# Optimization experiments

Measured on AMD Instinct MI355X. Metric: run time of the kernel, lower is better.

The kernel has to match this reference:

```python
import jax, jax.numpy as jnp
import numpy as np

DIM_IN, DIM_OUT, DIM_INNER = 1024, 1024, 128
SCALE = DIM_INNER ** -0.5


def setup_inputs() -> dict:
    key = jax.random.key(0)
    k1, k2, k3, k4 = jax.random.split(key, 4)
    x = jax.random.normal(k1, (4, 4096, DIM_IN), dtype=jnp.float32)
    # torch nn.Linear stores weight as [out, in]; we keep that layout and transpose in matmul
    w_qkv = jax.random.normal(k2, (3 * DIM_INNER, DIM_IN), dtype=jnp.float32) * (DIM_IN ** -0.5)
    w_out = jax.random.normal(k3, (DIM_OUT, DIM_INNER), dtype=jnp.float32) * (DIM_INNER ** -0.5)
    b_out = jax.random.normal(k4, (DIM_OUT,), dtype=jnp.float32) * 0.02
    return {"x": x, "w_qkv": w_qkv, "w_out": w_out, "b_out": b_out}


def reference(x, w_qkv, w_out, b_out):
    # qkv projection (no bias)
    qkv = jnp.einsum('bnd,ed->bne', x, w_qkv)            # [b, n, 3*dim_inner]
    q, k, v = jnp.split(qkv, 3, axis=-1)                 # each [b, n, dim_inner]
    sim = jnp.einsum('bid,bjd->bij', q, k) * SCALE       # [b, n, n]
    n = sim.shape[-1]
    causal = jnp.triu(jnp.ones((n, n), dtype=bool), 1)   # True above diagonal
    neg = jnp.finfo(q.dtype).max
    sim = jnp.where(causal[None, :, :], -neg, sim)
    attn = jax.nn.softmax(sim, axis=-1)
    out = jnp.einsum('bij,bjd->bid', attn, v)            # [b, n, dim_inner]
    return jnp.einsum('bnd,od->bno', out, w_out) + b_out # [b, n, dim_out]
```

## Files before the change

### kernel.cpp

```cpp
#include <hip/hip_runtime.h>
#include <math.h>


typedef __attribute__((ext_vector_type(8))) short bf16x8;
typedef __attribute__((ext_vector_type(4))) short bf16x4;
typedef __attribute__((ext_vector_type(4))) float f32x4;

#define FA_SCL2 0.12751886525137387f

__device__ __forceinline__ unsigned short f2bf(float f) {
    __bf16 h = (__bf16)f;
    return __builtin_bit_cast(unsigned short, h);
}
__device__ __forceinline__ float bf2f(unsigned short h) {
    union { unsigned u; float f; } v; v.u = ((unsigned)h) << 16;
    return v.f;
}
__device__ __forceinline__ f32x4 mfma16(bf16x8 a, bf16x8 b, f32x4 c) {
    return __builtin_amdgcn_mfma_f32_16x16x32_bf16(a, b, c, 0, 0, 0);
}
__device__ __forceinline__ void gl2lds16(const void* g, void* l) {
    __builtin_amdgcn_global_load_lds(
        (const __attribute__((address_space(1))) unsigned int*)g,
        (__attribute__((address_space(3))) unsigned int*)l, 16, 0, 0);
}
__device__ __forceinline__ f32x4 vmax4(f32x4 a, f32x4 b) {
    return f32x4{fmaxf(a[0], b[0]), fmaxf(a[1], b[1]),
                 fmaxf(a[2], b[2]), fmaxf(a[3], b[3])};
}

__global__ __launch_bounds__(256)
void wcast(const float* __restrict__ W, unsigned short* __restrict__ wfm)
{
    const int idx = blockIdx.x * 256 + threadIdx.x;
    const int kc = idx & 127, r = idx >> 7;
    const float* g = W + (size_t)r * 1024 + kc * 8;
    float4 w0 = *(const float4*)g, w1 = *(const float4*)(g + 4);
    bf16x8 p;
    p[0] = (short)f2bf(w0.x); p[1] = (short)f2bf(w0.y);
    p[2] = (short)f2bf(w0.z); p[3] = (short)f2bf(w0.w);
    p[4] = (short)f2bf(w1.x); p[5] = (short)f2bf(w1.y);
    p[6] = (short)f2bf(w1.z); p[7] = (short)f2bf(w1.w);
    *(bf16x8*)&wfm[(size_t)(kc * 384 + r) * 8] = p;
}

__global__ __launch_bounds__(256)
void woutcast(const float* __restrict__ W, unsigned short* __restrict__ wofm)
{
    const int idx = blockIdx.x * 256 + threadIdx.x;
    const int c = idx & 15, rg = idx >> 4;
    const float* g = W + (size_t)rg * 128 + c * 8;
    float4 w0 = *(const float4*)g, w1 = *(const float4*)(g + 4);
    bf16x8 p;
    p[0] = (short)f2bf(w0.x); p[1] = (short)f2bf(w0.y);
    p[2] = (short)f2bf(w0.z); p[3] = (short)f2bf(w0.w);
    p[4] = (short)f2bf(w1.x); p[5] = (short)f2bf(w1.y);
    p[6] = (short)f2bf(w1.z); p[7] = (short)f2bf(w1.w);
    *(bf16x8*)&wofm[((size_t)((rg >> 6) * 16 + c) * 64 + (rg & 63)) * 8] = p;
}

__global__ __launch_bounds__(512)
void gemm_qkv(const float* __restrict__ X, const unsigned short* __restrict__ Wfm,
              unsigned short* __restrict__ qfm, unsigned short* __restrict__ kfm,
              unsigned short* __restrict__ vpl)
{
    __shared__ unsigned short Asl[2048];
    __shared__ unsigned short Bsl[3][12288];
    const int tid = threadIdx.x;
    const int wv = tid >> 6, lane = tid & 63;
    const int lm = lane & 15, quad = lane >> 4;
    const int mb = blockIdx.x * 64;
    const int arow = tid >> 3, af4 = tid & 7;

    f32x4 acc[4][3];
    #pragma unroll
    for (int i = 0; i < 4; ++i)
        #pragma unroll
        for (int j = 0; j < 3; ++j) acc[i][j] = f32x4{0.f, 0.f, 0.f, 0.f};

    const float* gx = X + (size_t)(mb + arow) * 1024 + af4 * 4;

    auto issueB = [&](int it, int buf) {
        #pragma unroll
        for (int i = 0; i < 3; ++i) {
            const int p = wv * 3 + i;
            const int kcl = p & 3, rg = p >> 2;
            gl2lds16(Wfm + (size_t)((it * 4 + kcl) * 384 + rg * 64) * 8 + lane * 8,
                     &Bsl[buf][(kcl * 384 + rg * 64) * 8]);
        }
    };

    float4 f0 = *(const float4*)gx;
    issueB(0, 0);
    float4 f1 = *(const float4*)(gx + 32);
    issueB(1, 1);

    auto step = [&](const int i, float4& f) {
        __builtin_amdgcn_s_barrier();
        {
            bf16x4 pk;
            pk[0] = (short)f2bf(f.x); pk[1] = (short)f2bf(f.y);
            pk[2] = (short)f2bf(f.z); pk[3] = (short)f2bf(f.w);
            *(bf16x4*)&Asl[((af4 >> 1) * 64 + arow) * 8 + (af4 & 1) * 4] = pk;
        }
        if (i < 30) {
            f = *(const float4*)(gx + (i + 2) * 32);
            issueB(i + 2, (i + 2) % 3);
            asm volatile("s_waitcnt vmcnt(14) lgkmcnt(0)" ::: "memory");
        } else if (i == 30) {
            asm volatile("s_waitcnt vmcnt(7) lgkmcnt(0)" ::: "memory");
        } else {
            asm volatile("s_waitcnt vmcnt(0) lgkmcnt(0)" ::: "memory");
        }
        __builtin_amdgcn_s_barrier();
        const unsigned short* Bc = Bsl[i % 3];
        bf16x8 afr[4], bfr[3];
        #pragma unroll
        for (int i4 = 0; i4 < 4; ++i4)
            afr[i4] = *(const bf16x8*)&Asl[(quad * 64 + i4 * 16 + lm) * 8];
        #pragma unroll
        for (int j = 0; j < 3; ++j)
            bfr[j] = *(const bf16x8*)&Bc[(quad * 384 + wv * 48 + j * 16 + lm) * 8];
        #pragma unroll
        for (int i4 = 0; i4 < 4; ++i4)
            #pragma unroll
            for (int j = 0; j < 3; ++j)
                acc[i4][j] = mfma16(afr[i4], bfr[j], acc[i4][j]);
    };

    for (int p = 0; p < 16; ++p) { step(2 * p, f0); step(2 * p + 1, f1); }

    #pragma unroll
    for (int j = 0; j < 3; ++j) {
        const int ncg = wv * 48 + j * 16 + lm;
        const int sect = ncg >> 7, ncol = ncg & 127;
        if (sect == 2) {
            #pragma unroll
            for (int i = 0; i < 4; ++i)
                #pragma unroll
                for (int r = 0; r < 4; ++r)
                    vpl[(size_t)(mb + i * 16 + quad * 4 + r) * 128 + ncol]
                        = f2bf(acc[i][j][r]);
        } else {
            unsigned short* dst = sect ? kfm : qfm;
            const float scl = sect ? 1.f : FA_SCL2;
            const size_t cb = ((size_t)blockIdx.x * 16 + (ncol >> 3)) * 512 + (ncol & 7);
            #pragma unroll
            for (int i = 0; i < 4; ++i)
                #pragma unroll
                for (int r = 0; r < 4; ++r)
                    dst[cb + (size_t)(i * 16 + quad * 4 + r) * 8]
                        = f2bf(acc[i][j][r] * scl);
        }
    }
}

__global__ __launch_bounds__(256)
void transpose_v(const unsigned short* __restrict__ V, unsigned short* __restrict__ Vfm)
{
    __shared__ unsigned short T[128 * 72];
    const int tid = threadIdx.x;
    const int b  = blockIdx.x >> 6;
    const int kt = blockIdx.x & 63;
    const unsigned short* src = V + ((size_t)b * 4096 + kt * 64) * 128;
    #pragma unroll
    for (int i = 0; i < 4; ++i) {
        const int idx = tid + i * 256;
        const int key = idx >> 4, c8 = (idx & 15) * 8;
        bf16x8 d = *(const bf16x8*)(src + key * 128 + c8);
        #pragma unroll
        for (int e = 0; e < 8; ++e) T[(c8 + e) * 72 + key] = (unsigned short)d[e];
    }
    __syncthreads();
    unsigned short* dst = Vfm + (size_t)(b * 64 + kt) * 8192;
    #pragma unroll
    for (int i = 0; i < 4; ++i) {
        const int o = tid + i * 256;
        const int d = o & 127, c = o >> 7;
        bf16x8 x = *(const bf16x8*)&T[d * 72 + c * 8];
        *(bf16x8*)(dst + ((size_t)c * 128 + d) * 8) = x;
    }
}

__global__ __launch_bounds__(512)
void flash_attn3(const unsigned short* __restrict__ Qfm, const unsigned short* __restrict__ Kfm,
                 const unsigned short* __restrict__ Vfm,
                 unsigned short* __restrict__ Opart, float* __restrict__ Ml)
{
    __shared__ unsigned short Klds[2][8192];
    __shared__ unsigned short Vlds[2][8192];
    __shared__ unsigned short Plds[8][1024];

    const int tid = threadIdx.x;
    const int wv = tid >> 6, lane = tid & 63;
    const int lm = lane & 15, quad = lane >> 4;

    const int bx = blockIdx.x;
    const int xcd = bx & 7;
    const int b   = xcd >> 1;
    const int r   = (bx >> 3) * 2 + (xcd & 1);
    const int sp  = r & 3;
    const int Qi  = (r < 64) ? (16 + (r >> 2)) : (15 - ((r - 64) >> 2));
    const int n   = 2 * Qi + 2;
    const int cnt = (n >> 2) + ((sp < (n & 3)) ? 1 : 0);
    const int ktb = sp * (n >> 2) + ((sp < (n & 3)) ? sp : (n & 3));
    const int kte = ktb + cnt;
    const int qtw = 2 * Qi + (wv >> 2);
    const int rw  = (wv & 3) * 16;

    const int qt0 = 2 * Qi;
    const size_t ob0 = (size_t)((b * 64 + qt0) * 4 + sp) * 8192;
    const size_t ob1 = ob0 + 4 * 8192;
    const int mlb0 = ((b * 64 + qt0) * 4 + sp) * 128, mlb1 = mlb0 + 512;

    if (cnt == 0) {
        bf16x8 z = {0, 0, 0, 0, 0, 0, 0, 0};
        #pragma unroll
        for (int t = 0; t < 2; ++t) {
            *(bf16x8*)&Opart[ob0 + (size_t)(tid + t * 512) * 8] = z;
            *(bf16x8*)&Opart[ob1 + (size_t)(tid + t * 512) * 8] = z;
        }
        if (tid < 64) { Ml[mlb0 + tid] = -INFINITY; Ml[mlb1 + tid] = -INFINITY; }
        else if (tid < 128) { Ml[mlb0 + tid] = 0.f; Ml[mlb1 + tid] = 0.f; }
        return;
    }

    {
        const size_t qb = (size_t)(b * 64 + qt0) * 8192;
        #pragma unroll
        for (int i = 0; i < 4; ++i) {
            const int p = wv * 4 + i;
            gl2lds16(Qfm + qb + (size_t)p * 512 + lane * 8, &Klds[0][0] + p * 512);
        }
    }
    __syncthreads();
    bf16x8 qf[4];
    {
        const unsigned short* Qt = &Klds[wv >> 2][0];
        #pragma unroll
        for (int c = 0; c < 4; ++c)
            qf[c] = *(const bf16x8*)&Qt[((c * 4 + quad) * 64 + rw + lm) * 8];
    }
    asm volatile("s_waitcnt lgkmcnt(0)" ::: "memory");
    __builtin_amdgcn_s_barrier();

    {
        const size_t kb = (size_t)(b * 64 + ktb) * 8192;
        #pragma unroll
        for (int i = 0; i < 2; ++i) {
            const int pc = wv * 2 + i;
            gl2lds16(Kfm + kb + pc * 512 + lane * 8, &Klds[0][pc * 512]);
            gl2lds16(Vfm + kb + pc * 512 + lane * 8, &Vlds[0][pc * 512]);
        }
    }

    f32x4 oacc[8];
    #pragma unroll
    for (int oc = 0; oc < 8; ++oc) oacc[oc] = f32x4{0.f, 0.f, 0.f, 0.f};
    f32x4 m4 = f32x4{-INFINITY, -INFINITY, -INFINITY, -INFINITY};
    f32x4 lacc = f32x4{0.f, 0.f, 0.f, 0.f};
    unsigned short* Pw = Plds[wv];
    const short ONE = (short)0x3F80;
    const bf16x8 ONESB = {ONE, ONE, ONE, ONE, ONE, ONE, ONE, ONE};

    for (int kt = ktb; kt < kte; ++kt) {
        const int cu = (kt - ktb) & 1;
        __builtin_amdgcn_s_barrier();
        if (kt + 1 < kte) {
            const size_t kb = (size_t)(b * 64 + kt + 1) * 8192;
            #pragma unroll
            for (int i = 0; i < 2; ++i) {
                const int pc = wv * 2 + i;
                gl2lds16(Kfm + kb + pc * 512 + lane * 8, &Klds[cu ^ 1][pc * 512]);
                gl2lds16(Vfm + kb + pc * 512 + lane * 8, &Vlds[cu ^ 1][pc * 512]);
            }
            asm volatile("s_waitcnt vmcnt(4)" ::: "memory");
        } else {
            asm volatile("s_waitcnt vmcnt(0)" ::: "memory");
        }
        __builtin_amdgcn_s_barrier();
        if (kt > qtw) continue;

        const unsigned short* Kc = &Klds[cu][0];
        const unsigned short* Vc = &Vlds[cu][0];

        f32x4 sv[4];
        __builtin_amdgcn_s_setprio(1);
        #pragma unroll
        for (int ct = 0; ct < 4; ++ct) {
            f32x4 a = f32x4{0.f, 0.f, 0.f, 0.f};
            #pragma unroll
            for (int c = 0; c < 4; ++c) {
                bf16x8 kf = *(const bf16x8*)&Kc[((c * 4 + quad) * 64 + ct * 16 + lm) * 8];
                a = mfma16(qf[c], kf, a);
            }
            sv[ct] = a;
        }
        __builtin_amdgcn_s_setprio(0);
        if (kt == qtw) {
            #pragma unroll
            for (int ct = 0; ct < 4; ++ct) {
                const int dg = ct * 16 + lm - rw - quad * 4;
                #pragma unroll
                for (int rr = 0; rr < 4; ++rr)
                    if (dg > rr) sv[ct][rr] = -INFINITY;
            }
        }
        const f32x4 pmax = vmax4(vmax4(sv[0], sv[1]), vmax4(sv[2], sv[3]));
        const float dm = fmaxf(fmaxf(pmax[0] - m4[0], pmax[1] - m4[1]),
                               fmaxf(pmax[2] - m4[2], pmax[3] - m4[3]));
        if (!__all(dm <= 8.f)) {
            f32x4 rmax = pmax;
            #pragma unroll
            for (int d = 1; d < 16; d <<= 1) {
                f32x4 o;
                #pragma unroll
                for (int e = 0; e < 4; ++e) o[e] = __shfl_xor(rmax[e], d);
                rmax = vmax4(rmax, o);
            }
            const f32x4 mnew = vmax4(m4, rmax);
            f32x4 alpha;
            #pragma unroll
            for (int e = 0; e < 4; ++e) alpha[e] = __builtin_amdgcn_exp2f(m4[e] - mnew[e]);
            m4 = mnew;
            #pragma unroll
            for (int oc = 0; oc < 8; ++oc) oacc[oc] *= alpha;
            lacc *= alpha;
        }
        #pragma unroll
        for (int ct = 0; ct < 4; ++ct)
            #pragma unroll
            for (int rr = 0; rr < 4; ++rr)
                sv[ct][rr] = __builtin_amdgcn_exp2f(sv[ct][rr] - m4[rr]);
        #pragma unroll
        for (int ct = 0; ct < 4; ++ct) {
            const int cb = ((ct * 2 + (lm >> 3)) * 16 + quad * 4) * 8 + (lm & 7);
            #pragma unroll
            for (int rr = 0; rr < 4; ++rr)
                Pw[cb + rr * 8] = f2bf(sv[ct][rr]);
        }
        __builtin_amdgcn_s_setprio(1);
        #pragma unroll
        for (int s = 0; s < 2; ++s) {
            bf16x8 pf = *(const bf16x8*)&Pw[((s * 4 + quad) * 16 + lm) * 8];
            lacc = mfma16(pf, ONESB, lacc);
            #pragma unroll
            for (int oc = 0; oc < 8; ++oc) {
                bf16x8 vf = *(const bf16x8*)&Vc[((s * 4 + quad) * 128 + oc * 16 + lm) * 8];
                oacc[oc] = mfma16(pf, vf, oacc[oc]);
            }
        }
        __builtin_amdgcn_s_setprio(0);
    }

    const size_t obw = (size_t)((b * 64 + qtw) * 4 + sp) * 8192;
    const int mlw = ((b * 64 + qtw) * 4 + sp) * 128;
    #pragma unroll
    for (int oc = 0; oc < 8; ++oc) {
        const size_t cb = obw + (size_t)((oc * 2 + (lm >> 3)) * 64
                          + rw + quad * 4) * 8 + (lm & 7);
        #pragma unroll
        for (int rr = 0; rr < 4; ++rr)
            Opart[cb + rr * 8] = f2bf(oacc[oc][rr]);
    }
    if (lm == 0)
        #pragma unroll
        for (int rr = 0; rr < 4; ++rr) {
            const int row = rw + quad * 4 + rr;
            Ml[mlw + row] = m4[rr];
            Ml[mlw + 64 + row] = lacc[rr];
        }
}

__global__ __launch_bounds__(256)
void fa_combine(const unsigned short* __restrict__ Opart, const float* __restrict__ Ml,
                unsigned short* __restrict__ Ofm)
{
    const int bq = blockIdx.x;
    const int tid = threadIdx.x;
    const size_t pbase = (size_t)bq * 4 * 8192;
    const int mlb = bq * 4 * 128;
    #pragma unroll
    for (int t = 0; t < 4; ++t) {
        const int g = tid + t * 256;
        const int r = g & 63;
        float m[4], l[4];
        #pragma unroll
        for (int s = 0; s < 4; ++s) {
            m[s] = Ml[mlb + s * 128 + r];
            l[s] = Ml[mlb + s * 128 + 64 + r];
        }
        const float M = fmaxf(fmaxf(m[0], m[1]), fmaxf(m[2], m[3]));
        float a[4], den = 0.f;
        #pragma unroll
        for (int s = 0; s < 4; ++s) {
            a[s] = __builtin_amdgcn_exp2f(m[s] - M);
            den += a[s] * l[s];
        }
        const float rsc = 1.f / den;
        float acc[8] = {};
        #pragma unroll
        for (int s = 0; s < 4; ++s) {
            bf16x8 x = *(const bf16x8*)&Opart[pbase + (size_t)s * 8192 + (size_t)g * 8];
            #pragma unroll
            for (int e = 0; e < 8; ++e) acc[e] += a[s] * bf2f((unsigned short)x[e]);
        }
        bf16x8 o;
        #pragma unroll
        for (int e = 0; e < 8; ++e) o[e] = f2bf(acc[e] * rsc);
        *(bf16x8*)&Ofm[(size_t)bq * 8192 + (size_t)g * 8] = o;
    }
}

__global__ __launch_bounds__(256)
void gemm_out(const unsigned short* __restrict__ Ain, const unsigned short* __restrict__ Wofm,
              const float* __restrict__ bias, float* __restrict__ out)
{
    __shared__ unsigned short Bsl[16384];
    __shared__ unsigned short Asl[2][4096];
    const int tid = threadIdx.x;
    const int mb = blockIdx.x * 128;
    const int nb = blockIdx.y * 128;
    const int wv = tid >> 6, lane = tid & 63;
    const int wr = (wv >> 1) * 64, wc = (wv & 1) * 64;
    const int lm = lane & 15, quad = lane >> 4;

    #pragma unroll
    for (int i = 0; i < 8; ++i) {
        const int p = wv * 8 + i;
        gl2lds16(Wofm + (size_t)(((nb >> 6) + (p >> 4)) * 16 + (p & 15)) * 512 + lane * 8,
                 &Bsl[p * 512]);
    }
    #pragma unroll
    for (int i = 0; i < 2; ++i) {
        const int id = wv * 2 + i, t = id >> 2, kcl = id & 3;
        gl2lds16(Ain + (size_t)((mb >> 6) + t) * 8192 + kcl * 512 + lane * 8,
                 &Asl[0][(t * 4 + kcl) * 512]);
    }

    f32x4 acc[4][4];
    #pragma unroll
    for (int i = 0; i < 4; ++i)
        #pragma unroll
        for (int j = 0; j < 4; ++j) acc[i][j] = f32x4{0.f, 0.f, 0.f, 0.f};

    for (int kt = 0; kt < 4; ++kt) {
        __builtin_amdgcn_s_barrier();
        if (kt < 3) {
            #pragma unroll
            for (int i = 0; i < 2; ++i) {
                const int id = wv * 2 + i, t = id >> 2, kcl = id & 3;
                gl2lds16(Ain + (size_t)((mb >> 6) + t) * 8192 + ((kt + 1) * 4 + kcl) * 512 + lane * 8,
                         &Asl[(kt + 1) & 1][(t * 4 + kcl) * 512]);
            }
            asm volatile("s_waitcnt vmcnt(2)" ::: "memory");
        } else {
            asm volatile("s_waitcnt vmcnt(0)" ::: "memory");
        }
        __builtin_amdgcn_s_barrier();
        const unsigned short* Ac = Asl[kt & 1];
        bf16x8 af[4], bfr[4];
        #pragma unroll
        for (int i = 0; i < 4; ++i)
            af[i] = *(const bf16x8*)&Ac[(((wv >> 1) * 4 + quad) * 64 + i * 16 + lm) * 8];
        #pragma unroll
        for (int j = 0; j < 4; ++j)
            bfr[j] = *(const bf16x8*)&Bsl[(((wc >> 6) * 16 + kt * 4 + quad) * 64 + j * 16 + lm) * 8];
        #pragma unroll
        for (int i = 0; i < 4; ++i)
            #pragma unroll
            for (int j = 0; j < 4; ++j)
                acc[i][j] = mfma16(af[i], bfr[j], acc[i][j]);
    }

    #pragma unroll
    for (int j = 0; j < 4; ++j) {
        const int col = nb + wc + j * 16 + lm;
        const float bv = bias[col];
        #pragma unroll
        for (int i = 0; i < 4; ++i)
            #pragma unroll
            for (int r = 0; r < 4; ++r) {
                const int m = mb + wr + i * 16 + quad * 4 + r;
                out[(size_t)m * 1024 + col] = acc[i][j][r] + bv;
            }
    }
}

extern "C" void kernel_launch(void* const* d_in, const int* in_sizes, int n_in,
                              void* d_out, int out_size, void* d_ws, size_t ws_size,
                              hipStream_t stream)
{
    (void)in_sizes; (void)n_in; (void)out_size; (void)ws_size;
    const float* x     = (const float*)d_in[0];
    const float* w_qkv = (const float*)d_in[1];
    const float* w_out = (const float*)d_in[2];
    const float* b_out = (const float*)d_in[3];
    float* out = (float*)d_out;
    unsigned short* ws = (unsigned short*)d_ws;

    const size_t NE = (size_t)16384 * 128;
    unsigned short* qfm = ws;
    unsigned short* kfm = ws + NE;
    unsigned short* vpl = ws + 2 * NE;
    unsigned short* vfm = ws + 3 * NE;
    unsigned short* op  = ws + 4 * NE;
    float*          ml  = (float*)(ws + 8 * NE);
    unsigned short* ofm = qfm;
    unsigned short* wfm = op;
    unsigned short* wofm = vpl;

    hipLaunchKernelGGL(wcast,       dim3(192),    dim3(256), 0, stream, w_qkv, wfm);
    hipLaunchKernelGGL(gemm_qkv,    dim3(256),    dim3(512), 0, stream, x, wfm, qfm, kfm, vpl);
    hipLaunchKernelGGL(transpose_v, dim3(256),    dim3(256), 0, stream, vpl, vfm);
    hipLaunchKernelGGL(woutcast,    dim3(64),     dim3(256), 0, stream, w_out, wofm);
    hipLaunchKernelGGL(flash_attn3, dim3(512),    dim3(512), 0, stream, qfm, kfm, vfm, op, ml);
    hipLaunchKernelGGL(fa_combine,  dim3(256),    dim3(256), 0, stream, op, ml, ofm);
    hipLaunchKernelGGL(gemm_out,    dim3(128, 8), dim3(256), 0, stream, ofm, wofm, b_out, out);
}
```

Measured before the change: 198.2 us.

## Split QKV GEMM along N into two blocks per M tile and add occupancy hints

The QKV projection GEMM now launches 512 blocks of 256 threads instead of 256 blocks of 512 threads. Each block computes 192 of the 384 output columns, and each thread loads 8 floats of X per step instead of 4. This halves the LDS needed for the B tiles and doubles the number of blocks, so more CUs can be filled and occupancy can rise. The cost is that every X tile is now read and converted to bf16 twice. Launch-bound minimum-blocks hints are also added to the attention and output GEMM kernels, which may force register limits and spills.

Result: no change. 196.2 us (-1.0%).

```diff
diff --git a/kernel.cpp b/kernel.cpp
--- a/kernel.cpp
+++ b/kernel.cpp
@@ -59,18 +59,20 @@
     *(bf16x8*)&wofm[((size_t)((rg >> 6) * 16 + c) * 64 + (rg & 63)) * 8] = p;
 }
 
-__global__ __launch_bounds__(512)
+__global__ __launch_bounds__(256, 4)
 void gemm_qkv(const float* __restrict__ X, const unsigned short* __restrict__ Wfm,
               unsigned short* __restrict__ qfm, unsigned short* __restrict__ kfm,
               unsigned short* __restrict__ vpl)
 {
     __shared__ unsigned short Asl[2048];
-    __shared__ unsigned short Bsl[3][12288];
+    __shared__ unsigned short Bsl[3][6144];
     const int tid = threadIdx.x;
     const int wv = tid >> 6, lane = tid & 63;
     const int lm = lane & 15, quad = lane >> 4;
-    const int mb = blockIdx.x * 64;
-    const int arow = tid >> 3, af4 = tid & 7;
+    const int mt = blockIdx.x & 255;
+    const int nh = blockIdx.x >> 8;
+    const int mb = mt * 64, nb = nh * 192;
+    const int arow = tid >> 2, af4 = tid & 3;
 
     f32x4 acc[4][3];
     #pragma unroll
@@ -78,37 +80,42 @@
         #pragma unroll
         for (int j = 0; j < 3; ++j) acc[i][j] = f32x4{0.f, 0.f, 0.f, 0.f};
 
-    const float* gx = X + (size_t)(mb + arow) * 1024 + af4 * 4;
+    const float* gx = X + (size_t)(mb + arow) * 1024 + af4 * 8;
 
     auto issueB = [&](int it, int buf) {
         #pragma unroll
         for (int i = 0; i < 3; ++i) {
             const int p = wv * 3 + i;
             const int kcl = p & 3, rg = p >> 2;
-            gl2lds16(Wfm + (size_t)((it * 4 + kcl) * 384 + rg * 64) * 8 + lane * 8,
-                     &Bsl[buf][(kcl * 384 + rg * 64) * 8]);
+            gl2lds16(Wfm + ((size_t)((it * 4 + kcl) * 384) + nb + rg * 64) * 8 + lane * 8,
+                     &Bsl[buf][(kcl * 192 + rg * 64) * 8]);
         }
     };
 
-    float4 f0 = *(const float4*)gx;
+    float4 a00 = *(const float4*)gx;
+    float4 a01 = *(const float4*)(gx + 4);
     issueB(0, 0);
-    float4 f1 = *(const float4*)(gx + 32);
+    float4 a10 = *(const float4*)(gx + 32);
+    float4 a11 = *(const float4*)(gx + 36);
     issueB(1, 1);
 
-    auto step = [&](const int i, float4& f) {
+    auto step = [&](const int i, float4& fa, float4& fb) {
         __builtin_amdgcn_s_barrier();
         {
-            bf16x4 pk;
-            pk[0] = (short)f2bf(f.x); pk[1] = (short)f2bf(f.y);
-            pk[2] = (short)f2bf(f.z); pk[3] = (short)f2bf(f.w);
-            *(bf16x4*)&Asl[((af4 >> 1) * 64 + arow) * 8 + (af4 & 1) * 4] = pk;
+            bf16x8 pk;
+            pk[0] = (short)f2bf(fa.x); pk[1] = (short)f2bf(fa.y);
+            pk[2] = (short)f2bf(fa.z); pk[3] = (short)f2bf(fa.w);
+            pk[4] = (short)f2bf(fb.x); pk[5] = (short)f2bf(fb.y);
+            pk[6] = (short)f2bf(fb.z); pk[7] = (short)f2bf(fb.w);
+            *(bf16x8*)&Asl[(af4 * 64 + arow) * 8] = pk;
         }
         if (i < 30) {
-            f = *(const float4*)(gx + (i + 2) * 32);
+            fa = *(const float4*)(gx + (i + 2) * 32);
+            fb = *(const float4*)(gx + (i + 2) * 32 + 4);
             issueB(i + 2, (i + 2) % 3);
-            asm volatile("s_waitcnt vmcnt(14) lgkmcnt(0)" ::: "memory");
+            asm volatile("s_waitcnt vmcnt(10) lgkmcnt(0)" ::: "memory");
         } else if (i == 30) {
-            asm volatile("s_waitcnt vmcnt(7) lgkmcnt(0)" ::: "memory");
+            asm volatile("s_waitcnt vmcnt(5) lgkmcnt(0)" ::: "memory");
         } else {
             asm volatile("s_waitcnt vmcnt(0) lgkmcnt(0)" ::: "memory");
         }
@@ -120,7 +127,7 @@
             afr[i4] = *(const bf16x8*)&Asl[(quad * 64 + i4 * 16 + lm) * 8];
         #pragma unroll
         for (int j = 0; j < 3; ++j)
-            bfr[j] = *(const bf16x8*)&Bc[(quad * 384 + wv * 48 + j * 16 + lm) * 8];
+            bfr[j] = *(const bf16x8*)&Bc[(quad * 192 + wv * 48 + j * 16 + lm) * 8];
         #pragma unroll
         for (int i4 = 0; i4 < 4; ++i4)
             #pragma unroll
@@ -128,11 +135,11 @@
                 acc[i4][j] = mfma16(afr[i4], bfr[j], acc[i4][j]);
     };
 
-    for (int p = 0; p < 16; ++p) { step(2 * p, f0); step(2 * p + 1, f1); }
+    for (int p = 0; p < 16; ++p) { step(2 * p, a00, a01); step(2 * p + 1, a10, a11); }
 
     #pragma unroll
     for (int j = 0; j < 3; ++j) {
-        const int ncg = wv * 48 + j * 16 + lm;
+        const int ncg = nb + wv * 48 + j * 16 + lm;
         const int sect = ncg >> 7, ncol = ncg & 127;
         if (sect == 2) {
             #pragma unroll
@@ -144,7 +151,7 @@
         } else {
             unsigned short* dst = sect ? kfm : qfm;
             const float scl = sect ? 1.f : FA_SCL2;
-            const size_t cb = ((size_t)blockIdx.x * 16 + (ncol >> 3)) * 512 + (ncol & 7);
+            const size_t cb = ((size_t)mt * 16 + (ncol >> 3)) * 512 + (ncol & 7);
             #pragma unroll
             for (int i = 0; i < 4; ++i)
                 #pragma unroll
@@ -182,7 +189,7 @@
     }
 }
 
-__global__ __launch_bounds__(512)
+__global__ __launch_bounds__(512, 4)
 void flash_attn3(const unsigned short* __restrict__ Qfm, const unsigned short* __restrict__ Kfm,
                  const unsigned short* __restrict__ Vfm,
                  unsigned short* __restrict__ Opart, float* __restrict__ Ml)
@@ -412,7 +419,7 @@
     }
 }
 
-__global__ __launch_bounds__(256)
+__global__ __launch_bounds__(256, 4)
 void gemm_out(const unsigned short* __restrict__ Ain, const unsigned short* __restrict__ Wofm,
               const float* __restrict__ bias, float* __restrict__ out)
 {
@@ -511,7 +518,7 @@
     unsigned short* wofm = vpl;
 
     hipLaunchKernelGGL(wcast,       dim3(192),    dim3(256), 0, stream, w_qkv, wfm);
-    hipLaunchKernelGGL(gemm_qkv,    dim3(256),    dim3(512), 0, stream, x, wfm, qfm, kfm, vpl);
+    hipLaunchKernelGGL(gemm_qkv,    dim3(512),    dim3(256), 0, stream, x, wfm, qfm, kfm, vpl);
     hipLaunchKernelGGL(transpose_v, dim3(256),    dim3(256), 0, stream, vpl, vfm);
     hipLaunchKernelGGL(woutcast,    dim3(64),     dim3(256), 0, stream, w_out, wofm);
     hipLaunchKernelGGL(flash_attn3, dim3(512),    dim3(512), 0, stream, qfm, kfm, vfm, op, ml);
```
